# Optimization experiments

Hardware: AMD Instinct MI355X
Metric: run time of the kernel (lower is better)

## Reference

```python
import math
import jax, jax.numpy as jnp
from jax import lax
import numpy as np

NHEADS = 8
GN_GROUPS = 32
GN_EPS = 1e-5
L2_EPS = 1e-12


def conv2d(x, w, b=None, groups=1):
    # x: [B,C,H,W], w: [O, I/groups, kh, kw], stride 1, torch padding=k//2 (SAME)
    out = lax.conv_general_dilated(
        x, w, window_strides=(1, 1), padding='SAME',
        dimension_numbers=('NCHW', 'OIHW', 'NCHW'),
        feature_group_count=groups)
    if b is not None:
        out = out + b[None, :, None, None]
    return out


def group_norm(x, scale, bias, groups, eps=GN_EPS):
    B, C, H, W = x.shape
    xg = x.reshape(B, groups, C // groups, H, W)
    mu = jnp.mean(xg, axis=(2, 3, 4), keepdims=True)
    var = jnp.var(xg, axis=(2, 3, 4), keepdims=True)
    xg = (xg - mu) * lax.rsqrt(var + eps)
    x = xg.reshape(B, C, H, W)
    return x * scale[None, :, None, None] + bias[None, :, None, None]


def l2norm_ch(x):
    # F.normalize(x, dim=1): divide by channel L2 norm, clamped at eps
    n = jnp.sqrt(jnp.sum(x * x, axis=1, keepdims=True))
    return x / jnp.maximum(n, L2_EPS)


def attn_op(q, k, v, nheads, scale):
    # q,k,v: [B, C, xf, yf] real; tokens = frequency bins, features = C/nheads
    b, c, xf, yf = q.shape
    hd = c // nheads
    qh = q.reshape(b, nheads, hd, xf * yf)
    kh = k.reshape(b, nheads, hd, xf * yf)
    vh = v.reshape(b, nheads, hd, xf * yf)
    sim = jnp.einsum('bhcm,bhcn->bhmn', qh, kh) * scale
    attn = jax.nn.softmax(sim, axis=-1)
    out = jnp.einsum('bhmn,bhcn->bhcm', attn, vh)
    return out.reshape(b, c, xf, yf)


def setup_inputs() -> dict:
    key = jax.random.key(0)
    ks = jax.random.split(key, 14)
    B, H, W = 4, 48, 48
    fea = cond_c = qkv = dout = 256

    def rn(k, shape, s=0.05):
        return jax.random.normal(k, shape, dtype=jnp.float32) * s

    return {
        'x': jax.random.normal(ks[0], (B, fea, H, W), jnp.float32),
        'cond': jax.random.normal(ks[1], (B, cond_c, H, W), jnp.float32),
        'gn_w': jnp.ones((fea,), jnp.float32),
        'gn_b': jnp.zeros((fea,), jnp.float32),
        'q_dw': rn(ks[2], (fea, 1, 3, 3)),          # depthwise 3x3, groups=fea
        'q_pw_w': rn(ks[3], (qkv, fea, 1, 1)),
        'q_pw_b': jnp.zeros((qkv,), jnp.float32),
        'kv_dw': rn(ks[4], (cond_c, 1, 3, 3)),
        'kv_pw_w': rn(ks[5], (2 * qkv, cond_c, 1, 1)),
        'kv_pw_b': jnp.zeros((2 * qkv,), jnp.float32),
        'attn_out_w': rn(ks[6], (dout, qkv, 1, 1)),
        'attn_out_b': jnp.zeros((dout,), jnp.float32),
        'ffn_w1': rn(ks[7], (2 * dout, dout, 3, 3)),
        'ffn_w2': rn(ks[8], (dout, 2 * dout, 3, 3)),
        'ffn_w3': rn(ks[9], (dout, dout, 1, 1)),
        'ffn_b3': jnp.zeros((dout,), jnp.float32),
    }


def reference(x, cond, gn_w, gn_b, q_dw, q_pw_w, q_pw_b, kv_dw, kv_pw_w, kv_pw_b,
              attn_out_w, attn_out_b, ffn_w1, ffn_w2, ffn_w3, ffn_b3):
    B, C, H, W = x.shape
    qkv_dim = q_pw_w.shape[0]
    scale = 1.0 / math.sqrt(qkv_dim // NHEADS)

    xn = group_norm(x, gn_w, gn_b, GN_GROUPS)
    q = conv2d(conv2d(xn, q_dw, groups=C), q_pw_w, q_pw_b)
    kv = conv2d(conv2d(cond, kv_dw, groups=cond.shape[1]), kv_pw_w, kv_pw_b)
    k, v = jnp.split(kv, 2, axis=1)
    q, k, v = l2norm_ch(q), l2norm_ch(k), l2norm_ch(v)

    qf = jnp.fft.rfft2(q, axes=(-2, -1), norm='ortho')
    kf = jnp.fft.rfft2(k, axes=(-2, -1), norm='ortho')
    vf = jnp.fft.rfft2(v, axes=(-2, -1), norm='ortho')

    amp = attn_op(jnp.abs(qf), jnp.abs(kf), jnp.abs(vf), NHEADS, scale)
    phas = attn_op(jnp.angle(qf), jnp.angle(kf), jnp.angle(vf), NHEADS, scale)
    outc = lax.complex(amp * jnp.cos(phas), amp * jnp.sin(phas))  # torch.polar
    out = jnp.fft.irfft2(outc, s=(H, W), axes=(-2, -1), norm='ortho')

    attn_out = conv2d(out, attn_out_w, attn_out_b) + xn  # attn_res = Identity (fea_dim == dim_out)
    h1 = jax.nn.silu(conv2d(attn_out, ffn_w1))
    h2 = conv2d(h1, ffn_w2)
    ffn = conv2d(h2, ffn_w3, ffn_b3)
    # DropPath is identity in eval mode
    return ffn + attn_out
```

## Files before the change

### kernel.cpp

```cpp
#include <hip/hip_runtime.h>
#include <hip/hip_bf16.h>
#include <math.h>

constexpr int Bn = 4, Cn = 256, Hn = 48, Wn = 48, HW = 2304;
constexpr float ATT_SCALE = 0.17677669529663687f;

typedef __attribute__((ext_vector_type(8))) short bf16x8;
typedef __attribute__((ext_vector_type(4))) float f32x4;

#define MFMA16(A, B, C) __builtin_amdgcn_mfma_f32_16x16x32_bf16(A, B, C, 0, 0, 0)

__global__ void gn_kernel(const float* __restrict__ x, const float* __restrict__ gw,
                          const float* __restrict__ gb, float* __restrict__ y) {
  int bg = blockIdx.x;
  const float* xp = x + (size_t)bg * 18432;
  float* yp = y + (size_t)bg * 18432;
  float s = 0.f, ss = 0.f;
  for (int i = threadIdx.x; i < 18432; i += 256) { float v = xp[i]; s += v; ss += v * v; }
#pragma unroll
  for (int off = 32; off; off >>= 1) { s += __shfl_xor(s, off); ss += __shfl_xor(ss, off); }
  __shared__ float rs[4], rss[4];
  int wid = threadIdx.x >> 6;
  if ((threadIdx.x & 63) == 0) { rs[wid] = s; rss[wid] = ss; }
  __syncthreads();
  s = rs[0] + rs[1] + rs[2] + rs[3];
  ss = rss[0] + rss[1] + rss[2] + rss[3];
  float mean = s * (1.f / 18432.f);
  float var = ss * (1.f / 18432.f) - mean * mean;
  float inv = rsqrtf(var + 1e-5f);
  int g = bg & 31;
  for (int i = threadIdx.x; i < 18432; i += 256) {
    int c = (g << 3) + (i / 2304);
    yp[i] = (xp[i] - mean) * inv * gw[c] + gb[c];
  }
}

__global__ void dw3x3_kernel(const float* __restrict__ in, const float* __restrict__ wd,
                             float* __restrict__ out) {
  int bc = blockIdx.x;
  int c = bc & 255;
  const float* ip = in + (size_t)bc * HW;
  float* op = out + (size_t)bc * HW;
  float w[9];
#pragma unroll
  for (int k = 0; k < 9; ++k) w[k] = wd[c * 9 + k];
  for (int p = threadIdx.x; p < HW; p += 256) {
    int yy = p / 48, xx = p - yy * 48;
    float a = 0.f;
#pragma unroll
    for (int ky = 0; ky < 3; ++ky) {
      int y2 = yy + ky - 1;
      if ((unsigned)y2 < 48u) {
#pragma unroll
        for (int kx = 0; kx < 3; ++kx) {
          int x2 = xx + kx - 1;
          if ((unsigned)x2 < 48u) a += ip[y2 * 48 + x2] * w[ky * 3 + kx];
        }
      }
    }
    op[p] = a;
  }
}

__global__ void wt_kernel(const float* __restrict__ w, float* __restrict__ wt, int O) {
  int q = blockIdx.x * 256 + threadIdx.x;
  int c = q / O, o = q - c * O;
  wt[q] = w[(size_t)o * 256 + c];
}

template <bool RES>
__global__ void __launch_bounds__(256)
pw2_kernel(const float* __restrict__ in, size_t in_bs, const float* __restrict__ WT,
           const float* __restrict__ bias, const float* __restrict__ res, size_t res_bs,
           float* __restrict__ out, size_t out_bs, int CO) {
  __shared__ float sx[32][260];
  __shared__ float swt[32][36];
  const int tid = threadIdx.x;
  const int px0 = blockIdx.x * 256;
  const int ob = blockIdx.y * 32;
  const int img = blockIdx.z;
  const int wv = tid >> 6, pxl = tid & 63;
  const float* ip = in + (size_t)img * in_bs + px0;

  float4 acc[8];
#pragma unroll
  for (int j = 0; j < 8; ++j) acc[j] = make_float4(0.f, 0.f, 0.f, 0.f);

  for (int c0 = 0; c0 < 256; c0 += 32) {
    __syncthreads();
#pragma unroll
    for (int i = 0; i < 8; ++i) {
      int q = tid + i * 256;
      int c = q >> 6, f4 = q & 63;
      *(float4*)&sx[c][f4 * 4] = *(const float4*)(ip + (size_t)(c0 + c) * HW + f4 * 4);
    }
    {
      int c = tid >> 3, f = tid & 7;
      *(float4*)&swt[c][f * 4] = *(const float4*)(WT + (size_t)(c0 + c) * CO + ob + f * 4);
    }
    __syncthreads();
#pragma unroll 4
    for (int c = 0; c < 32; ++c) {
      float4 xv = *(const float4*)&sx[c][pxl * 4];
      float4 wa = *(const float4*)&swt[c][wv * 8];
      float4 wb = *(const float4*)&swt[c][wv * 8 + 4];
      float w8[8] = {wa.x, wa.y, wa.z, wa.w, wb.x, wb.y, wb.z, wb.w};
#pragma unroll
      for (int j = 0; j < 8; ++j) {
        acc[j].x += w8[j] * xv.x; acc[j].y += w8[j] * xv.y;
        acc[j].z += w8[j] * xv.z; acc[j].w += w8[j] * xv.w;
      }
    }
  }

#pragma unroll
  for (int j = 0; j < 8; ++j) {
    int o = ob + wv * 8 + j;
    float4 a = acc[j];
    float bv = bias[o];
    a.x += bv; a.y += bv; a.z += bv; a.w += bv;
    if (RES) {
      float4 rv = *(const float4*)(res + (size_t)img * res_bs + (size_t)o * HW + px0 + pxl * 4);
      a.x += rv.x; a.y += rv.y; a.z += rv.z; a.w += rv.w;
    }
    *(float4*)(out + (size_t)img * out_bs + (size_t)o * HW + px0 + pxl * 4) = a;
  }
}

__global__ void l2n_kernel(float* __restrict__ t, size_t bstride) {
  int pxl = threadIdx.x & 63;
  int cg = threadIdx.x >> 6;
  int p = blockIdx.x * 64 + pxl;
  float* q = t + (size_t)blockIdx.y * bstride + p;
  float ss = 0.f;
#pragma unroll 8
  for (int c = cg * 64; c < cg * 64 + 64; ++c) { float v = q[(size_t)c * HW]; ss += v * v; }
  __shared__ float part[4][64];
  __shared__ float sinv[64];
  part[cg][pxl] = ss;
  __syncthreads();
  if (threadIdx.x < 64) {
    float tot = part[0][pxl] + part[1][pxl] + part[2][pxl] + part[3][pxl];
    sinv[pxl] = 1.f / fmaxf(sqrtf(tot), 1e-12f);
  }
  __syncthreads();
  float inv = sinv[pxl];
#pragma unroll 8
  for (int c = cg * 64; c < cg * 64 + 64; ++c) q[(size_t)c * HW] *= inv;
}

__global__ void dftmat_kernel(__hip_bfloat16* __restrict__ mt) {
  int t = blockIdx.x * 256 + threadIdx.x;
  const float TP = 6.283185307179586f;
  if (t < 4096) {
    int up = t >> 6, w = t & 63;
    float v = 0.f;
    if (w < 48 && up < 50) {
      int u = (up < 25) ? up : up - 25;
      float ang = TP * (float)((w * u) % 48) / 48.f;
      v = ((up < 25) ? cosf(ang) : -sinf(ang)) * (1.f / 48.f);
    }
    __hip_bfloat16 h = __float2bfloat16(v);
    mt[t] = h; mt[4096 + t] = __float2bfloat16(v - __bfloat162float(h));
  } else if (t < 7168) {
    int q = t - 4096;
    int vv = q >> 6, h = q & 63;
    float c = 0.f, s = 0.f;
    if (h < 48) {
      float ang = TP * (float)((vv * h) % 48) / 48.f;
      c = cosf(ang); s = sinf(ang);
    }
    __hip_bfloat16 ch = __float2bfloat16(c);
    mt[8192 + q] = ch; mt[11264 + q] = __float2bfloat16(c - __bfloat162float(ch));
    __hip_bfloat16 sh = __float2bfloat16(s);
    mt[14336 + q] = sh; mt[17408 + q] = __float2bfloat16(s - __bfloat162float(sh));
  } else if (t < 8704) {
    int q = t - 7168;
    int w = q >> 5, u = q & 31;
    float c = 0.f, s = 0.f;
    if (u < 25) {
      float ang = TP * (float)((u * w) % 48) / 48.f;
      c = cosf(ang); s = -sinf(ang);
    }
    __hip_bfloat16 ch = __float2bfloat16(c);
    mt[20480 + q] = ch; mt[22016 + q] = __float2bfloat16(c - __bfloat162float(ch));
    __hip_bfloat16 sh = __float2bfloat16(s);
    mt[23552 + q] = sh; mt[25088 + q] = __float2bfloat16(s - __bfloat162float(sh));
  }
}

template <bool TLAY>
__global__ void __launch_bounds__(256)
rfft2_mfma(const float* __restrict__ in, size_t bstride, const __hip_bfloat16* __restrict__ mt,
           __hip_bfloat16* __restrict__ amp, __hip_bfloat16* __restrict__ pha) {
  const int bc = blockIdx.x;
  const int bi = bc >> 8, ch = bc & 255;
  const float* ip = in + (size_t)bi * bstride + (size_t)ch * HW;
  __shared__ __align__(16) __hip_bfloat16 XH[48 * 72], XL[48 * 72];
  __shared__ __align__(16) __hip_bfloat16 Yt[4][32 * 72];
  const int tid = threadIdx.x;
  const int lane = tid & 63, lm = lane & 15, kg = lane >> 4, wv = tid >> 6;

  for (int i = tid; i < 48 * 72; i += 256) {
    int r = i / 72, w = i - r * 72;
    float v = (w < 48) ? ip[r * 48 + w] : 0.f;
    __hip_bfloat16 h = __float2bfloat16(v);
    XH[i] = h;
    XL[i] = __float2bfloat16(v - __bfloat162float(h));
  }
  for (int i = tid; i < 4 * 32 * 72; i += 256) ((unsigned short*)Yt)[i] = 0;
  __syncthreads();

  {
    const __hip_bfloat16* W1TH = mt;
    const __hip_bfloat16* W1TL = mt + 4096;
    const int brow = wv * 16 + lm;
    bf16x8 BH0 = *(const bf16x8*)(W1TH + brow * 64 + kg * 8);
    bf16x8 BH1 = *(const bf16x8*)(W1TH + brow * 64 + 32 + kg * 8);
    bf16x8 BL0 = *(const bf16x8*)(W1TL + brow * 64 + kg * 8);
    bf16x8 BL1 = *(const bf16x8*)(W1TL + brow * 64 + 32 + kg * 8);
#pragma unroll
    for (int mtI = 0; mtI < 3; ++mtI) {
      f32x4 acc = {0.f, 0.f, 0.f, 0.f};
      bf16x8 AH = *(const bf16x8*)(&XH[(mtI * 16 + lm) * 72 + kg * 8]);
      bf16x8 AL = *(const bf16x8*)(&XL[(mtI * 16 + lm) * 72 + kg * 8]);
      acc = MFMA16(AH, BH0, acc); acc = MFMA16(AH, BL0, acc); acc = MFMA16(AL, BH0, acc);
      AH = *(const bf16x8*)(&XH[(mtI * 16 + lm) * 72 + 32 + kg * 8]);
      AL = *(const bf16x8*)(&XL[(mtI * 16 + lm) * 72 + 32 + kg * 8]);
      acc = MFMA16(AH, BH1, acc); acc = MFMA16(AH, BL1, acc); acc = MFMA16(AL, BH1, acc);
      if (brow < 50) {
        int aidx = (brow < 25) ? 0 : 2;
        int u = (brow < 25) ? brow : brow - 25;
#pragma unroll
        for (int r = 0; r < 4; ++r) {
          int h = mtI * 16 + kg * 4 + r;
          float v = acc[r];
          __hip_bfloat16 hh = __float2bfloat16(v);
          Yt[aidx][u * 72 + h] = hh;
          Yt[aidx + 1][u * 72 + h] = __float2bfloat16(v - __bfloat162float(hh));
        }
      }
    }
  }
  __syncthreads();

  {
    const __hip_bfloat16* M2CH = mt + 8192;
    const __hip_bfloat16* M2CL = mt + 11264;
    const __hip_bfloat16* M2SH = mt + 14336;
    const __hip_bfloat16* M2SL = mt + 17408;
    for (int t = wv; t < 6; t += 4) {
      int mtI = t >> 1, ntI = t & 1;
      f32x4 aC1 = {0.f,0.f,0.f,0.f}, aS1 = {0.f,0.f,0.f,0.f};
      f32x4 aC2 = {0.f,0.f,0.f,0.f}, aS2 = {0.f,0.f,0.f,0.f};
#pragma unroll
      for (int ks = 0; ks < 2; ++ks) {
        int arow = mtI * 16 + lm;
        int k0 = ks * 32 + kg * 8;
        bf16x8 CH = *(const bf16x8*)(M2CH + arow * 64 + k0);
        bf16x8 CL = *(const bf16x8*)(M2CL + arow * 64 + k0);
        bf16x8 SH = *(const bf16x8*)(M2SH + arow * 64 + k0);
        bf16x8 SL = *(const bf16x8*)(M2SL + arow * 64 + k0);
        int brow = ntI * 16 + lm;
        bf16x8 ReH = *(const bf16x8*)(&Yt[0][brow * 72 + k0]);
        bf16x8 ReL = *(const bf16x8*)(&Yt[1][brow * 72 + k0]);
        bf16x8 ImH = *(const bf16x8*)(&Yt[2][brow * 72 + k0]);
        bf16x8 ImL = *(const bf16x8*)(&Yt[3][brow * 72 + k0]);
        aC1 = MFMA16(CH, ReH, aC1); aC1 = MFMA16(CH, ReL, aC1); aC1 = MFMA16(CL, ReH, aC1);
        aS2 = MFMA16(SH, ImH, aS2); aS2 = MFMA16(SH, ImL, aS2); aS2 = MFMA16(SL, ImH, aS2);
        aC2 = MFMA16(CH, ImH, aC2); aC2 = MFMA16(CH, ImL, aC2); aC2 = MFMA16(CL, ImH, aC2);
        aS1 = MFMA16(SH, ReH, aS1); aS1 = MFMA16(SH, ReL, aS1); aS1 = MFMA16(SL, ReH, aS1);
      }
      int u = ntI * 16 + lm;
      if (u < 25) {
#pragma unroll
        for (int r = 0; r < 4; ++r) {
          int v = mtI * 16 + kg * 4 + r;
          float zre = aC1[r] + aS2[r];
          float zim = aC2[r] - aS1[r];
          float am = sqrtf(zre * zre + zim * zim);
          float ph = atan2f(zim, zre);
          int i = v * 25 + u;
          size_t o;
          if (TLAY) o = ((size_t)(bc >> 5) * 1200 + i) * 32 + (bc & 31);
          else      o = (size_t)bc * 1200 + i;
          amp[o] = __float2bfloat16(am);
          pha[o] = __float2bfloat16(ph);
        }
      }
    }
  }
}

__global__ void __launch_bounds__(256)
polar_irfft2_mfma(const float* __restrict__ amp, const float* __restrict__ pha,
                  const __hip_bfloat16* __restrict__ mt, float* __restrict__ out) {
  const int bc = blockIdx.x;
  __shared__ __align__(16) __hip_bfloat16 Zt[4][32 * 72];
  __shared__ __align__(16) __hip_bfloat16 Yp[4][48 * 56];
  const int tid = threadIdx.x;
  const int lane = tid & 63, lm = lane & 15, kg = lane >> 4, wv = tid >> 6;

  for (int i = tid; i < 4 * 32 * 72; i += 256) ((unsigned short*)Zt)[i] = 0;
  for (int i = tid; i < 4 * 48 * 56; i += 256) ((unsigned short*)Yp)[i] = 0;
  __syncthreads();
  for (int i = tid; i < 1200; i += 256) {
    int v = i / 25, u = i - v * 25;
    float a = amp[(size_t)bc * 1200 + i];
    float p = pha[(size_t)bc * 1200 + i];
    float sc = (u == 0 || u == 24) ? (1.f / 48.f) : (2.f / 48.f);
    float zre = a * cosf(p) * sc;
    float zim = a * sinf(p) * sc;
    __hip_bfloat16 h0 = __float2bfloat16(zre);
    Zt[0][u * 72 + v] = h0;
    Zt[1][u * 72 + v] = __float2bfloat16(zre - __bfloat162float(h0));
    __hip_bfloat16 h1 = __float2bfloat16(zim);
    Zt[2][u * 72 + v] = h1;
    Zt[3][u * 72 + v] = __float2bfloat16(zim - __bfloat162float(h1));
  }
  __syncthreads();

  {
    const __hip_bfloat16* M2CH = mt + 8192;
    const __hip_bfloat16* M2CL = mt + 11264;
    const __hip_bfloat16* M2SH = mt + 14336;
    const __hip_bfloat16* M2SL = mt + 17408;
    for (int t = wv; t < 6; t += 4) {
      int mtI = t >> 1, ntI = t & 1;
      f32x4 aC1 = {0.f,0.f,0.f,0.f}, aS1 = {0.f,0.f,0.f,0.f};
      f32x4 aC2 = {0.f,0.f,0.f,0.f}, aS2 = {0.f,0.f,0.f,0.f};
#pragma unroll
      for (int ks = 0; ks < 2; ++ks) {
        int arow = mtI * 16 + lm;
        int k0 = ks * 32 + kg * 8;
        bf16x8 CH = *(const bf16x8*)(M2CH + arow * 64 + k0);
        bf16x8 CL = *(const bf16x8*)(M2CL + arow * 64 + k0);
        bf16x8 SH = *(const bf16x8*)(M2SH + arow * 64 + k0);
        bf16x8 SL = *(const bf16x8*)(M2SL + arow * 64 + k0);
        int brow = ntI * 16 + lm;
        bf16x8 ReH = *(const bf16x8*)(&Zt[0][brow * 72 + k0]);
        bf16x8 ReL = *(const bf16x8*)(&Zt[1][brow * 72 + k0]);
        bf16x8 ImH = *(const bf16x8*)(&Zt[2][brow * 72 + k0]);
        bf16x8 ImL = *(const bf16x8*)(&Zt[3][brow * 72 + k0]);
        aC1 = MFMA16(CH, ReH, aC1); aC1 = MFMA16(CH, ReL, aC1); aC1 = MFMA16(CL, ReH, aC1);
        aS2 = MFMA16(SH, ImH, aS2); aS2 = MFMA16(SH, ImL, aS2); aS2 = MFMA16(SL, ImH, aS2);
        aC2 = MFMA16(CH, ImH, aC2); aC2 = MFMA16(CH, ImL, aC2); aC2 = MFMA16(CL, ImH, aC2);
        aS1 = MFMA16(SH, ReH, aS1); aS1 = MFMA16(SH, ReL, aS1); aS1 = MFMA16(SL, ReH, aS1);
      }
      int u = ntI * 16 + lm;
      if (u < 25) {
#pragma unroll
        for (int r = 0; r < 4; ++r) {
          int h = mtI * 16 + kg * 4 + r;
          float yre = aC1[r] - aS2[r];
          float yim = aS1[r] + aC2[r];
          __hip_bfloat16 h0 = __float2bfloat16(yre);
          Yp[0][h * 56 + u] = h0;
          Yp[1][h * 56 + u] = __float2bfloat16(yre - __bfloat162float(h0));
          __hip_bfloat16 h1 = __float2bfloat16(yim);
          Yp[2][h * 56 + u] = h1;
          Yp[3][h * 56 + u] = __float2bfloat16(yim - __bfloat162float(h1));
        }
      }
    }
  }
  __syncthreads();

  {
    const __hip_bfloat16* W3CH = mt + 20480;
    const __hip_bfloat16* W3CL = mt + 22016;
    const __hip_bfloat16* W3SH = mt + 23552;
    const __hip_bfloat16* W3SL = mt + 25088;
    for (int t = wv; t < 9; t += 4) {
      int mtI = t / 3, ntI = t - (t / 3) * 3;
      f32x4 acc = {0.f, 0.f, 0.f, 0.f};
      int k0 = kg * 8;
      bf16x8 AH = *(const bf16x8*)(&Yp[0][(mtI * 16 + lm) * 56 + k0]);
      bf16x8 AL = *(const bf16x8*)(&Yp[1][(mtI * 16 + lm) * 56 + k0]);
      bf16x8 IH = *(const bf16x8*)(&Yp[2][(mtI * 16 + lm) * 56 + k0]);
      bf16x8 IL = *(const bf16x8*)(&Yp[3][(mtI * 16 + lm) * 56 + k0]);
      int brow = ntI * 16 + lm;
      bf16x8 CH = *(const bf16x8*)(W3CH + brow * 32 + k0);
      bf16x8 CL = *(const bf16x8*)(W3CL + brow * 32 + k0);
      bf16x8 SH = *(const bf16x8*)(W3SH + brow * 32 + k0);
      bf16x8 SL = *(const bf16x8*)(W3SL + brow * 32 + k0);
      acc = MFMA16(AH, CH, acc); acc = MFMA16(AH, CL, acc); acc = MFMA16(AL, CH, acc);
      acc = MFMA16(IH, SH, acc); acc = MFMA16(IH, SL, acc); acc = MFMA16(IL, SH, acc);
#pragma unroll
      for (int r = 0; r < 4; ++r) {
        int h = mtI * 16 + kg * 4 + r;
        out[(size_t)bc * 2304 + h * 48 + brow] = acc[r];
      }
    }
  }
}

__global__ void __launch_bounds__(64)
attn_mfma(const __hip_bfloat16* __restrict__ Qt, const __hip_bfloat16* __restrict__ Kt,
          const __hip_bfloat16* __restrict__ Vc, float* __restrict__ Om) {
  const int bh = blockIdx.y;
  const int m0 = blockIdx.x * 16;
  const int lane = threadIdx.x;
  const int lm = lane & 15, kg = lane >> 4;
  __shared__ unsigned short Pl[16][40];
  __shared__ float linv[16];
  const __hip_bfloat16* Qp = Qt + ((size_t)bh * 1200 + m0) * 32;
  const __hip_bfloat16* Kp = Kt + (size_t)bh * 38400;
  const __hip_bfloat16* Vp = Vc + (size_t)bh * 38400;
  const bf16x8 qf = *(const bf16x8*)(Qp + lm * 32 + kg * 8);

  float mx = -3.0e38f;
  for (int n0 = 0; n0 < 1200; n0 += 16) {
    bf16x8 kf = *(const bf16x8*)(Kp + (size_t)(n0 + lm) * 32 + kg * 8);
    f32x4 d = {0.f, 0.f, 0.f, 0.f};
    d = MFMA16(kf, qf, d);
    mx = fmaxf(mx, fmaxf(fmaxf(d[0], d[1]), fmaxf(d[2], d[3])));
  }
  mx = fmaxf(mx, __shfl_xor(mx, 16));
  mx = fmaxf(mx, __shfl_xor(mx, 32));
  const float Cs = ATT_SCALE * 1.44269504f;
  const float mxl = mx * Cs;

  f32x4 acc0 = {0.f, 0.f, 0.f, 0.f}, acc1 = {0.f, 0.f, 0.f, 0.f};
  float psum = 0.f;
  for (int g = 0; g < 38; ++g) {
    const int n0 = g * 32;
#pragma unroll
    for (int t = 0; t < 2; ++t) {
      const int nn = n0 + t * 16;
      ushort4 pk;
      if (nn < 1200) {
        bf16x8 kf = *(const bf16x8*)(Kp + (size_t)(nn + lm) * 32 + kg * 8);
        f32x4 d = {0.f, 0.f, 0.f, 0.f};
        d = MFMA16(kf, qf, d);
        float p0 = exp2f(d[0] * Cs - mxl), p1 = exp2f(d[1] * Cs - mxl);
        float p2 = exp2f(d[2] * Cs - mxl), p3 = exp2f(d[3] * Cs - mxl);
        psum += p0 + p1 + p2 + p3;
        pk.x = __builtin_bit_cast(unsigned short, __float2bfloat16(p0));
        pk.y = __builtin_bit_cast(unsigned short, __float2bfloat16(p1));
        pk.z = __builtin_bit_cast(unsigned short, __float2bfloat16(p2));
        pk.w = __builtin_bit_cast(unsigned short, __float2bfloat16(p3));
      } else {
        pk.x = pk.y = pk.z = pk.w = 0;
      }
      *(ushort4*)(&Pl[lm][t * 16 + kg * 4]) = pk;
    }
    bf16x8 pa = *(const bf16x8*)(&Pl[lm][kg * 8]);
    bf16x8 v0 = *(const bf16x8*)(Vp + (size_t)lm * 1200 + n0 + kg * 8);
    bf16x8 v1 = *(const bf16x8*)(Vp + (size_t)(16 + lm) * 1200 + n0 + kg * 8);
    acc0 = MFMA16(pa, v0, acc0);
    acc1 = MFMA16(pa, v1, acc1);
  }
  psum += __shfl_xor(psum, 16);
  psum += __shfl_xor(psum, 32);
  if (kg == 0) linv[lm] = 1.f / psum;
  __syncthreads();
#pragma unroll
  for (int r = 0; r < 4; ++r) {
    int m = m0 + kg * 4 + r;
    float li = linv[kg * 4 + r];
    Om[(size_t)bh * 38400 + (size_t)lm * 1200 + m] = acc0[r] * li;
    Om[(size_t)bh * 38400 + (size_t)(16 + lm) * 1200 + m] = acc1[r] * li;
  }
}

__global__ void packx_kernel(const float* __restrict__ in, __hip_bfloat16* __restrict__ xp) {
  int y = blockIdx.x;
  int b = blockIdx.y;
  int c = threadIdx.x;
  const float* ip = in + ((size_t)(b * 256 + c) * 48 + y) * 48;
  __hip_bfloat16* op = xp + ((size_t)(b * 8 + (c >> 5)) * 2500 + (size_t)(y + 1) * 50 + 1) * 32 + (c & 31);
  for (int x = 0; x < 48; ++x) op[x * 32] = __float2bfloat16(ip[x]);
}

template <int CIN>
__global__ void packw_kernel(const float* __restrict__ w, __hip_bfloat16* __restrict__ wp, int O) {
  int t = blockIdx.x * 256 + threadIdx.x;
  int o = t / CIN, c = t - o * CIN;
  if (o >= O) return;
  constexpr int NC = CIN / 32;
#pragma unroll
  for (int tap = 0; tap < 9; ++tap)
    wp[(((size_t)tap * NC + (c >> 5)) * O + o) * 32 + (c & 31)] = __float2bfloat16(w[(size_t)t * 9 + tap]);
}

__global__ void addf4_kernel(float* __restrict__ a, const float* __restrict__ b) {
  int i = blockIdx.x * 256 + threadIdx.x;
  float4 x = ((float4*)a)[i];
  float4 y = ((const float4*)b)[i];
  x.x += y.x; x.y += y.y; x.z += y.z; x.w += y.w;
  ((float4*)a)[i] = x;
}

template <int CIN, int CO, bool TO_PAD, int KS>
__global__ void __launch_bounds__(256)
mfconv3x3(const __hip_bfloat16* __restrict__ Xp, const __hip_bfloat16* __restrict__ Wp,
          __hip_bfloat16* __restrict__ Op, float* __restrict__ Of) {
  constexpr int NC = CIN / 32;
  constexpr int KC = NC / KS;
  constexpr int MT = CO / 32;
  const int q = gridDim.x >> 3;
  const int swz = (blockIdx.x & 7) * q + (blockIdx.x >> 3);
  const int mt = swz % MT;
  const int ks = (swz / MT) % KS;
  const int rq = swz / (MT * KS);
  const int img = rq / 12;
  const int y0b = (rq % 12) * 4;
  const int tid = threadIdx.x;
  const int wv = tid >> 6;
  const int y = y0b + wv;
  const int lane = tid & 63;
  const int lm = lane & 15, kg = lane >> 4;
  const int o0 = mt * 32;
  const int ci0 = ks * KC;

  __shared__ __hip_bfloat16 Als[9216];
  __shared__ __hip_bfloat16 Bls[9600];

  f32x4 acc[2][3];
#pragma unroll
  for (int f = 0; f < 2; ++f)
#pragma unroll
    for (int g = 0; g < 3; ++g) acc[f][g] = (f32x4){0.f, 0.f, 0.f, 0.f};

  for (int ci = 0; ci < KC; ++ci) {
    const int cic = ci0 + ci;
    const size_t wst = ((size_t)cic * CO + o0) * 32;
    const size_t bst = ((size_t)(img * NC + cic) * 2500 + (size_t)y0b * 50) * 32;
    __syncthreads();
    for (int c = tid; c < 2352; c += 256) {
      if (c < 1152) {
        int tap = c >> 7, rem = c & 127;
        float4 v = *(const float4*)(Wp + wst + (size_t)tap * (NC * CO * 32) + rem * 8);
        *(float4*)(&Als[c * 8]) = v;
      } else {
        int c2 = c - 1152;
        float4 v = *(const float4*)(Xp + bst + (size_t)c2 * 8);
        *(float4*)(&Bls[c2 * 8]) = v;
      }
    }
    __syncthreads();
#pragma unroll
    for (int tap = 0; tap < 9; ++tap) {
      const int dy = tap / 3 - 1, dx = tap - (tap / 3) * 3 - 1;
      bf16x8 A0 = *(const bf16x8*)(&Als[tap * 1024 + lm * 32 + kg * 8]);
      bf16x8 A1 = *(const bf16x8*)(&Als[tap * 1024 + 512 + lm * 32 + kg * 8]);
      const int bbase = ((wv + 1 + dy) * 50 + 1 + dx + lm) * 32 + kg * 8;
      bf16x8 B0 = *(const bf16x8*)(&Bls[bbase]);
      bf16x8 B1 = *(const bf16x8*)(&Bls[bbase + 512]);
      bf16x8 B2 = *(const bf16x8*)(&Bls[bbase + 1024]);
      acc[0][0] = MFMA16(A0, B0, acc[0][0]);
      acc[0][1] = MFMA16(A0, B1, acc[0][1]);
      acc[0][2] = MFMA16(A0, B2, acc[0][2]);
      acc[1][0] = MFMA16(A1, B0, acc[1][0]);
      acc[1][1] = MFMA16(A1, B1, acc[1][1]);
      acc[1][2] = MFMA16(A1, B2, acc[1][2]);
    }
  }

  if (TO_PAD) {
    const int cio = o0 >> 5;
#pragma unroll
    for (int f = 0; f < 2; ++f) {
      const int cc = f * 16 + kg * 4;
#pragma unroll
      for (int g = 0; g < 3; ++g) {
        int x = g * 16 + lm;
        ushort4 st;
        float v0 = acc[f][g][0], v1 = acc[f][g][1], v2 = acc[f][g][2], v3 = acc[f][g][3];
        v0 = v0 / (1.f + __expf(-v0)); v1 = v1 / (1.f + __expf(-v1));
        v2 = v2 / (1.f + __expf(-v2)); v3 = v3 / (1.f + __expf(-v3));
        st.x = __builtin_bit_cast(unsigned short, __float2bfloat16(v0));
        st.y = __builtin_bit_cast(unsigned short, __float2bfloat16(v1));
        st.z = __builtin_bit_cast(unsigned short, __float2bfloat16(v2));
        st.w = __builtin_bit_cast(unsigned short, __float2bfloat16(v3));
        *(ushort4*)(Op + (((size_t)(img * (CO / 32) + cio) * 2500 + (size_t)(y + 1) * 50 + (x + 1)) * 32 + cc)) = st;
      }
    }
  } else {
    float* Ofp = Of + (size_t)ks * 4 * CO * HW;
#pragma unroll
    for (int f = 0; f < 2; ++f)
#pragma unroll
      for (int g = 0; g < 3; ++g) {
        int x = g * 16 + lm;
#pragma unroll
        for (int r = 0; r < 4; ++r) {
          int o = o0 + f * 16 + kg * 4 + r;
          Ofp[((size_t)img * CO + o) * HW + y * 48 + x] = acc[f][g][r];
        }
      }
  }
}

extern "C" void kernel_launch(void* const* d_in, const int* in_sizes, int n_in,
                              void* d_out, int out_size, void* d_ws, size_t ws_size,
                              hipStream_t stream) {
  (void)in_sizes; (void)n_in; (void)out_size; (void)ws_size;
  const float* x      = (const float*)d_in[0];
  const float* cond   = (const float*)d_in[1];
  const float* gn_w   = (const float*)d_in[2];
  const float* gn_b   = (const float*)d_in[3];
  const float* q_dw   = (const float*)d_in[4];
  const float* q_pw_w = (const float*)d_in[5];
  const float* q_pw_b = (const float*)d_in[6];
  const float* kv_dw  = (const float*)d_in[7];
  const float* kv_pw_w= (const float*)d_in[8];
  const float* kv_pw_b= (const float*)d_in[9];
  const float* ao_w   = (const float*)d_in[10];
  const float* ao_b   = (const float*)d_in[11];
  const float* w1     = (const float*)d_in[12];
  const float* w2     = (const float*)d_in[13];
  const float* w3     = (const float*)d_in[14];
  const float* b3     = (const float*)d_in[15];
  float* ws = (float*)d_ws;
  float* Yo = (float*)d_out;

  const size_t U = 2359296;
  const size_t Hf = 1228800;
  const size_t CS = 589824;
  const size_t CS2 = 1179648;

  float* XN  = ws;
  float* DW  = ws + U;
  float* Qb  = ws + 2 * U;
  float* KV  = ws + 3 * U;
  __hip_bfloat16* AQT = (__hip_bfloat16*)(ws + 5 * U);
  __hip_bfloat16* PQT = AQT + 1228800;
  __hip_bfloat16* AKT = AQT + 2 * 1228800;
  __hip_bfloat16* PKT = AQT + 3 * 1228800;
  __hip_bfloat16* AVc = AQT + 4 * 1228800;
  __hip_bfloat16* PVc = AQT + 5 * 1228800;
  float* AO  = ws + 5 * U + 3 * Hf;
  float* PO  = AO + Hf;
  float* OUT = ws + U;
  float* ATT = ws + 5 * U;
  __hip_bfloat16* Xp1 = (__hip_bfloat16*)(ws + U);
  __hip_bfloat16* Xp2 = (__hip_bfloat16*)(ws + 2 * U);
  __hip_bfloat16* Wp1 = (__hip_bfloat16*)(ws + 2 * U + 2600000);
  __hip_bfloat16* Wp2 = (__hip_bfloat16*)(ws + 2 * U + 3200000);
  float* H2  = ws;
  float* H2b = ws + U;
  float* WTq  = ws + 5 * U + 5 * Hf;
  float* WTkv = WTq + 65536;
  float* WTao = WTkv + 131072;
  float* WT3  = WTao + 65536;
  __hip_bfloat16* MT = (__hip_bfloat16*)(WT3 + 65536);

  wt_kernel<<<256, 256, 0, stream>>>(q_pw_w, WTq, 256);
  wt_kernel<<<512, 256, 0, stream>>>(kv_pw_w, WTkv, 512);
  wt_kernel<<<256, 256, 0, stream>>>(ao_w, WTao, 256);
  wt_kernel<<<256, 256, 0, stream>>>(w3, WT3, 256);
  dftmat_kernel<<<34, 256, 0, stream>>>(MT);
  gn_kernel<<<128, 256, 0, stream>>>(x, gn_w, gn_b, XN);
  dw3x3_kernel<<<1024, 256, 0, stream>>>(XN, q_dw, DW);
  pw2_kernel<false><<<dim3(9, 8, 4), 256, 0, stream>>>(DW, CS, WTq, q_pw_b, nullptr, 0, Qb, CS, 256);
  dw3x3_kernel<<<1024, 256, 0, stream>>>(cond, kv_dw, DW);
  pw2_kernel<false><<<dim3(9, 16, 4), 256, 0, stream>>>(DW, CS, WTkv, kv_pw_b, nullptr, 0, KV, CS2, 512);
  l2n_kernel<<<dim3(36, 4), 256, 0, stream>>>(Qb, CS);
  l2n_kernel<<<dim3(36, 4), 256, 0, stream>>>(KV, CS2);
  l2n_kernel<<<dim3(36, 4), 256, 0, stream>>>(KV + CS, CS2);
  rfft2_mfma<true ><<<1024, 256, 0, stream>>>(Qb, CS, MT, AQT, PQT);
  rfft2_mfma<true ><<<1024, 256, 0, stream>>>(KV, CS2, MT, AKT, PKT);
  rfft2_mfma<false><<<1024, 256, 0, stream>>>(KV + CS, CS2, MT, AVc, PVc);
  attn_mfma<<<dim3(75, 32), 64, 0, stream>>>(AQT, AKT, AVc, AO);
  attn_mfma<<<dim3(75, 32), 64, 0, stream>>>(PQT, PKT, PVc, PO);
  polar_irfft2_mfma<<<1024, 256, 0, stream>>>(AO, PO, MT, OUT);
  pw2_kernel<true><<<dim3(9, 8, 4), 256, 0, stream>>>(OUT, CS, WTao, ao_b, XN, CS, ATT, CS, 256);
  hipMemsetAsync(Xp1, 0, 2560000 * sizeof(__hip_bfloat16), stream);
  hipMemsetAsync(Xp2, 0, 5120000 * sizeof(__hip_bfloat16), stream);
  packx_kernel<<<dim3(48, 4), 256, 0, stream>>>(ATT, Xp1);
  packw_kernel<256><<<512, 256, 0, stream>>>(w1, Wp1, 512);
  packw_kernel<512><<<512, 256, 0, stream>>>(w2, Wp2, 256);
  mfconv3x3<256, 512, true, 1><<<768, 256, 0, stream>>>(Xp1, Wp1, Xp2, nullptr);
  mfconv3x3<512, 256, false, 2><<<768, 256, 0, stream>>>(Xp2, Wp2, nullptr, H2);
  addf4_kernel<<<2304, 256, 0, stream>>>(H2, H2b);
  pw2_kernel<true><<<dim3(9, 8, 4), 256, 0, stream>>>(H2, CS, WT3, b3, ATT, CS, Yo, CS, 256);
}
```

Baseline: 528.7 us.

## Run pointwise convs on bf16x3 split-precision MFMA instead of fp32 FMA

Replaces the fp32 SIMT 1x1 convolution kernel with an MFMA kernel that splits inputs and weights into bf16 high/low parts and accumulates three products to keep near-fp32 accuracy. Weight preprocessing now packs hi/lo bf16 tiles in a K-blocked layout instead of transposing fp32. Each block computes all 256 output channels for 128 pixels, which cuts grid size sharply and may underfill the GPU; weights are streamed from global/L2 per wave rather than shared through LDS.

```diff
diff --git a/kernel.cpp b/kernel.cpp
--- a/kernel.cpp
+++ b/kernel.cpp
@@ -62,68 +62,85 @@
   }
 }
 
-__global__ void wt_kernel(const float* __restrict__ w, float* __restrict__ wt, int O) {
+__global__ void pwpack_kernel(const float* __restrict__ w, __hip_bfloat16* __restrict__ WH,
+                              __hip_bfloat16* __restrict__ WL, int O) {
   int q = blockIdx.x * 256 + threadIdx.x;
-  int c = q / O, o = q - c * O;
-  wt[q] = w[(size_t)o * 256 + c];
+  int o = q >> 8, c = q & 255;
+  float v = w[q];
+  __hip_bfloat16 h = __float2bfloat16(v);
+  size_t idx = ((size_t)(c >> 5) * O + o) * 32 + (c & 31);
+  WH[idx] = h;
+  WL[idx] = __float2bfloat16(v - __bfloat162float(h));
 }
 
 template <bool RES>
 __global__ void __launch_bounds__(256)
-pw2_kernel(const float* __restrict__ in, size_t in_bs, const float* __restrict__ WT,
-           const float* __restrict__ bias, const float* __restrict__ res, size_t res_bs,
-           float* __restrict__ out, size_t out_bs, int CO) {
-  __shared__ float sx[32][260];
-  __shared__ float swt[32][36];
+pw3_kernel(const float* __restrict__ in, size_t in_bs, const __hip_bfloat16* __restrict__ WH,
+           const __hip_bfloat16* __restrict__ WL, const float* __restrict__ bias,
+           const float* __restrict__ res, size_t res_bs, float* __restrict__ out,
+           size_t out_bs, int CO) {
+  __shared__ __align__(16) __hip_bfloat16 XH[128 * 40], XL[128 * 40];
   const int tid = threadIdx.x;
-  const int px0 = blockIdx.x * 256;
-  const int ob = blockIdx.y * 32;
+  const int px0 = blockIdx.x * 128;
+  const int ob = blockIdx.y * 256;
   const int img = blockIdx.z;
-  const int wv = tid >> 6, pxl = tid & 63;
-  const float* ip = in + (size_t)img * in_bs + px0;
-
-  float4 acc[8];
-#pragma unroll
-  for (int j = 0; j < 8; ++j) acc[j] = make_float4(0.f, 0.f, 0.f, 0.f);
+  const int wv = tid >> 6, lane = tid & 63, lm = lane & 15, kg = lane >> 4;
+
+  f32x4 acc[16][2];
+#pragma unroll
+  for (int mt = 0; mt < 16; ++mt) {
+    acc[mt][0] = (f32x4){0.f, 0.f, 0.f, 0.f};
+    acc[mt][1] = (f32x4){0.f, 0.f, 0.f, 0.f};
+  }
+
+  const int spx = tid & 127, sg = tid >> 7;
+  const float* ipb = in + (size_t)img * in_bs + px0 + spx;
 
   for (int c0 = 0; c0 < 256; c0 += 32) {
     __syncthreads();
-#pragma unroll
-    for (int i = 0; i < 8; ++i) {
-      int q = tid + i * 256;
-      int c = q >> 6, f4 = q & 63;
-      *(float4*)&sx[c][f4 * 4] = *(const float4*)(ip + (size_t)(c0 + c) * HW + f4 * 4);
-    }
     {
-      int c = tid >> 3, f = tid & 7;
-      *(float4*)&swt[c][f * 4] = *(const float4*)(WT + (size_t)(c0 + c) * CO + ob + f * 4);
+      const float* ip = ipb + (size_t)(c0 + sg * 16) * HW;
+#pragma unroll
+      for (int cc = 0; cc < 16; ++cc) {
+        float v = ip[(size_t)cc * HW];
+        __hip_bfloat16 h = __float2bfloat16(v);
+        XH[spx * 40 + sg * 16 + cc] = h;
+        XL[spx * 40 + sg * 16 + cc] = __float2bfloat16(v - __bfloat162float(h));
+      }
     }
     __syncthreads();
-#pragma unroll 4
-    for (int c = 0; c < 32; ++c) {
-      float4 xv = *(const float4*)&sx[c][pxl * 4];
-      float4 wa = *(const float4*)&swt[c][wv * 8];
-      float4 wb = *(const float4*)&swt[c][wv * 8 + 4];
-      float w8[8] = {wa.x, wa.y, wa.z, wa.w, wb.x, wb.y, wb.z, wb.w};
-#pragma unroll
-      for (int j = 0; j < 8; ++j) {
-        acc[j].x += w8[j] * xv.x; acc[j].y += w8[j] * xv.y;
-        acc[j].z += w8[j] * xv.z; acc[j].w += w8[j] * xv.w;
-      }
-    }
-  }
-
-#pragma unroll
-  for (int j = 0; j < 8; ++j) {
-    int o = ob + wv * 8 + j;
-    float4 a = acc[j];
-    float bv = bias[o];
-    a.x += bv; a.y += bv; a.z += bv; a.w += bv;
-    if (RES) {
-      float4 rv = *(const float4*)(res + (size_t)img * res_bs + (size_t)o * HW + px0 + pxl * 4);
-      a.x += rv.x; a.y += rv.y; a.z += rv.z; a.w += rv.w;
-    }
-    *(float4*)(out + (size_t)img * out_bs + (size_t)o * HW + px0 + pxl * 4) = a;
+    const int prow = (wv * 32 + lm) * 40 + kg * 8;
+    bf16x8 BH0 = *(const bf16x8*)(&XH[prow]);
+    bf16x8 BL0 = *(const bf16x8*)(&XL[prow]);
+    bf16x8 BH1 = *(const bf16x8*)(&XH[prow + 640]);
+    bf16x8 BL1 = *(const bf16x8*)(&XL[prow + 640]);
+    const size_t wb0 = ((size_t)(c0 >> 5) * CO + ob + lm) * 32 + kg * 8;
+#pragma unroll
+    for (int mt = 0; mt < 16; ++mt) {
+      bf16x8 AH = *(const bf16x8*)(WH + wb0 + (size_t)mt * 512);
+      bf16x8 AL = *(const bf16x8*)(WL + wb0 + (size_t)mt * 512);
+      acc[mt][0] = MFMA16(AH, BH0, acc[mt][0]);
+      acc[mt][0] = MFMA16(AH, BL0, acc[mt][0]);
+      acc[mt][0] = MFMA16(AL, BH0, acc[mt][0]);
+      acc[mt][1] = MFMA16(AH, BH1, acc[mt][1]);
+      acc[mt][1] = MFMA16(AH, BL1, acc[mt][1]);
+      acc[mt][1] = MFMA16(AL, BH1, acc[mt][1]);
+    }
+  }
+
+#pragma unroll
+  for (int mt = 0; mt < 16; ++mt) {
+#pragma unroll
+    for (int nt = 0; nt < 2; ++nt) {
+      int px = px0 + wv * 32 + nt * 16 + lm;
+#pragma unroll
+      for (int r = 0; r < 4; ++r) {
+        int o = ob + mt * 16 + kg * 4 + r;
+        float v = acc[mt][nt][r] + bias[o];
+        if (RES) v += res[(size_t)img * res_bs + (size_t)o * HW + px];
+        out[(size_t)img * out_bs + (size_t)o * HW + px] = v;
+      }
+    }
   }
 }
 
@@ -641,22 +658,23 @@
   __hip_bfloat16* Wp2 = (__hip_bfloat16*)(ws + 2 * U + 3200000);
   float* H2  = ws;
   float* H2b = ws + U;
-  float* WTq  = ws + 5 * U + 5 * Hf;
-  float* WTkv = WTq + 65536;
-  float* WTao = WTkv + 131072;
-  float* WT3  = WTao + 65536;
-  __hip_bfloat16* MT = (__hip_bfloat16*)(WT3 + 65536);
-
-  wt_kernel<<<256, 256, 0, stream>>>(q_pw_w, WTq, 256);
-  wt_kernel<<<512, 256, 0, stream>>>(kv_pw_w, WTkv, 512);
-  wt_kernel<<<256, 256, 0, stream>>>(ao_w, WTao, 256);
-  wt_kernel<<<256, 256, 0, stream>>>(w3, WT3, 256);
+  __hip_bfloat16* BW = (__hip_bfloat16*)(ws + 5 * U + 5 * Hf);
+  __hip_bfloat16* QWH = BW,            * QWL = BW + 65536;
+  __hip_bfloat16* KWH = BW + 131072,   * KWL = BW + 262144;
+  __hip_bfloat16* AWH = BW + 393216,   * AWL = BW + 458752;
+  __hip_bfloat16* W3H = BW + 524288,   * W3L = BW + 589824;
+  __hip_bfloat16* MT  = BW + 655360;
+
+  pwpack_kernel<<<256, 256, 0, stream>>>(q_pw_w, QWH, QWL, 256);
+  pwpack_kernel<<<512, 256, 0, stream>>>(kv_pw_w, KWH, KWL, 512);
+  pwpack_kernel<<<256, 256, 0, stream>>>(ao_w, AWH, AWL, 256);
+  pwpack_kernel<<<256, 256, 0, stream>>>(w3, W3H, W3L, 256);
   dftmat_kernel<<<34, 256, 0, stream>>>(MT);
   gn_kernel<<<128, 256, 0, stream>>>(x, gn_w, gn_b, XN);
   dw3x3_kernel<<<1024, 256, 0, stream>>>(XN, q_dw, DW);
-  pw2_kernel<false><<<dim3(9, 8, 4), 256, 0, stream>>>(DW, CS, WTq, q_pw_b, nullptr, 0, Qb, CS, 256);
+  pw3_kernel<false><<<dim3(18, 1, 4), 256, 0, stream>>>(DW, CS, QWH, QWL, q_pw_b, nullptr, 0, Qb, CS, 256);
   dw3x3_kernel<<<1024, 256, 0, stream>>>(cond, kv_dw, DW);
-  pw2_kernel<false><<<dim3(9, 16, 4), 256, 0, stream>>>(DW, CS, WTkv, kv_pw_b, nullptr, 0, KV, CS2, 512);
+  pw3_kernel<false><<<dim3(18, 2, 4), 256, 0, stream>>>(DW, CS, KWH, KWL, kv_pw_b, nullptr, 0, KV, CS2, 512);
   l2n_kernel<<<dim3(36, 4), 256, 0, stream>>>(Qb, CS);
   l2n_kernel<<<dim3(36, 4), 256, 0, stream>>>(KV, CS2);
   l2n_kernel<<<dim3(36, 4), 256, 0, stream>>>(KV + CS, CS2);
@@ -666,7 +684,7 @@
   attn_mfma<<<dim3(75, 32), 64, 0, stream>>>(AQT, AKT, AVc, AO);
   attn_mfma<<<dim3(75, 32), 64, 0, stream>>>(PQT, PKT, PVc, PO);
   polar_irfft2_mfma<<<1024, 256, 0, stream>>>(AO, PO, MT, OUT);
-  pw2_kernel<true><<<dim3(9, 8, 4), 256, 0, stream>>>(OUT, CS, WTao, ao_b, XN, CS, ATT, CS, 256);
+  pw3_kernel<true><<<dim3(18, 1, 4), 256, 0, stream>>>(OUT, CS, AWH, AWL, ao_b, XN, CS, ATT, CS, 256);
   hipMemsetAsync(Xp1, 0, 2560000 * sizeof(__hip_bfloat16), stream);
   hipMemsetAsync(Xp2, 0, 5120000 * sizeof(__hip_bfloat16), stream);
   packx_kernel<<<dim3(48, 4), 256, 0, stream>>>(ATT, Xp1);
@@ -675,5 +693,5 @@
   mfconv3x3<256, 512, true, 1><<<768, 256, 0, stream>>>(Xp1, Wp1, Xp2, nullptr);
   mfconv3x3<512, 256, false, 2><<<768, 256, 0, stream>>>(Xp2, Wp2, nullptr, H2);
   addf4_kernel<<<2304, 256, 0, stream>>>(H2, H2b);
-  pw2_kernel<true><<<dim3(9, 8, 4), 256, 0, stream>>>(H2, CS, WT3, b3, ATT, CS, Yo, CS, 256);
-}
+  pw3_kernel<true><<<dim3(18, 1, 4), 256, 0, stream>>>(H2, CS, W3H, W3L, b3, ATT, CS, Yo, CS, 256);
+}
```

Result: slower. 546.3 us (+3.3%).
